# Kernel optimization log

Measured on AMD Instinct MI355X. Metric: run time of the kernel, lower is better.

The kernel has to match this reference:

```python
import jax, jax.numpy as jnp
import numpy as np

B, T, H, K = 256, 1024, 12, 6
EPS = 1e-5


def _lstm_layer(x, Wih, Whh, bih, bhh):
    # x: [B, T, H]; torch gate order i, f, g, o
    b = bih + bhh

    def step(carry, xt):
        h, c = carry
        gates = xt @ Wih.T + h @ Whh.T + b
        i, f, g, o = jnp.split(gates, 4, axis=-1)
        c = jax.nn.sigmoid(f) * c + jax.nn.sigmoid(i) * jnp.tanh(g)
        h = jax.nn.sigmoid(o) * jnp.tanh(c)
        return (h, c), h

    h0 = jnp.zeros((x.shape[0], H), x.dtype)
    (_, _), ys = jax.lax.scan(step, (h0, h0), jnp.swapaxes(x, 0, 1))
    return jnp.swapaxes(ys, 0, 1)


def _bn_per_step(x, gamma, beta):
    # BatchNorm1d applied independently at each timestep (training mode):
    # normalize over the batch axis for each (t, channel).
    mu = jnp.mean(x, axis=0, keepdims=True)
    var = jnp.mean((x - mu) ** 2, axis=0, keepdims=True)  # biased, as torch BN
    return gamma * (x - mu) * jax.lax.rsqrt(var + EPS) + beta


def setup_inputs() -> dict:
    key = jax.random.key(0)
    ks = jax.random.split(key, 12)
    s = 1.0 / np.sqrt(H)
    return {
        "mfcc": jax.random.normal(ks[0], (B, T, H), jnp.float32),
        "Wih": jax.random.uniform(ks[1], (3, 4 * H, H), jnp.float32, -s, s),
        "Whh": jax.random.uniform(ks[2], (3, 4 * H, H), jnp.float32, -s, s),
        "bih": jax.random.uniform(ks[3], (3, 4 * H), jnp.float32, -s, s),
        "bhh": jax.random.uniform(ks[4], (3, 4 * H), jnp.float32, -s, s),
        "fc1_w": jax.random.normal(ks[5], (64, H), jnp.float32) * 0.1,
        "fc1_b": jnp.zeros((64,), jnp.float32),
        "bn1_g": jnp.ones((64,), jnp.float32),
        "bn1_b": jnp.zeros((64,), jnp.float32),
        "fc2_w": jax.random.normal(ks[6], (128, 64), jnp.float32) * 0.1,
        "fc2_b": jnp.zeros((128,), jnp.float32),
        "bn2_g": jnp.ones((128,), jnp.float32),
        "bn2_b": jnp.zeros((128,), jnp.float32),
        "fc3_w": jax.random.normal(ks[7], (K, 128), jnp.float32) * 0.1,
        "fc3_b": jnp.zeros((K,), jnp.float32),
        "WI": jax.random.normal(ks[8], (K, H, H), jnp.float32) * 0.01,
    }


def reference(mfcc, Wih, Whh, bih, bhh, fc1_w, fc1_b, bn1_g, bn1_b,
              fc2_w, fc2_b, bn2_g, bn2_b, fc3_w, fc3_b, WI):
    # 3-layer LSTM, input/hidden = 12
    x = mfcc
    for l in range(3):
        x = _lstm_layer(x, Wih[l], Whh[l], bih[l], bhh[l])

    # per-timestep MLP with per-timestep BatchNorm (training-mode stats)
    h = jnp.einsum('bth,oh->bto', x, fc1_w) + fc1_b
    h = jax.nn.relu(_bn_per_step(h, bn1_g, bn1_b))
    h = jnp.einsum('bth,oh->bto', h, fc2_w) + fc2_b
    h = jax.nn.relu(_bn_per_step(h, bn2_g, bn2_b))
    lambs = jnp.einsum('bth,kh->btk', h, fc3_w) + fc3_b  # [B, T, K]

    # out[b,t] = mfcc[b,t] @ (I + sum_k lambs[b,t,k] * WI[k])
    #          = mfcc[b,t] + sum_k lambs[b,t,k] * (mfcc[b,t] @ WI[k])
    proj = jnp.einsum('btd,kde->btke', mfcc, WI)  # [B, T, K, 12]
    outs = mfcc + jnp.einsum('btk,btke->bte', lambs, proj)
    return outs[:, None, :, :]  # [B, 1, T, 12]
```

## Files before the change

### kernel.cpp

```cpp
#include <hip/hip_runtime.h>

#define T_LEN 1024
#define NBATCH 256
#define HDIM 12
#define PAIR_STRIDE 12288
#define X3_TB 16

typedef __fp16 fp16x2 __attribute__((ext_vector_type(2)));

#if __has_builtin(__builtin_amdgcn_exp2f)
#define EXP2F(x) __builtin_amdgcn_exp2f(x)
#else
#define EXP2F(x) exp2f(x)
#endif
#if __has_builtin(__builtin_amdgcn_rcpf)
#define RCPF(x) __builtin_amdgcn_rcpf(x)
#else
#define RCPF(x) (1.0f / (x))
#endif

#define KSIG -1.4426950408889634f
#define KTAN -2.8853900817779268f

__device__ __forceinline__ unsigned bperm(int byteidx, unsigned v) {
#if __has_builtin(__builtin_amdgcn_ds_bpermute)
  return (unsigned)__builtin_amdgcn_ds_bpermute(byteidx, (int)v);
#else
  return (unsigned)__shfl((int)v, byteidx >> 2, 64);
#endif
}

template <int Q>
__device__ __forceinline__ float qb(float v) {
#if __has_builtin(__builtin_amdgcn_mov_dpp)
  return __int_as_float(__builtin_amdgcn_mov_dpp(__float_as_int(v), Q * 0x55, 0xF, 0xF, true));
#else
  return __shfl(v, (threadIdx.x & ~3) | Q, 64);
#endif
}

__device__ __forceinline__ float row_shr4(float v) {
#if __has_builtin(__builtin_amdgcn_mov_dpp)
  return __int_as_float(__builtin_amdgcn_mov_dpp(__float_as_int(v), 0x114, 0xF, 0xF, true));
#else
  return __shfl(v, (threadIdx.x & 63) - 4, 64);
#endif
}

__device__ __forceinline__ float h16tof(unsigned short u) {
  union { unsigned short s; _Float16 h; } c; c.s = u; return (float)c.h;
}
__device__ __forceinline__ unsigned short f16bits(float f) {
  union { unsigned short s; _Float16 h; } c; c.h = (_Float16)f; return c.s;
}
__device__ __forceinline__ float h16lo(unsigned u) {
  union { unsigned short s; _Float16 h; } c; c.s = (unsigned short)(u & 0xffffu); return (float)c.h;
}
__device__ __forceinline__ float h16hi(unsigned u) {
  union { unsigned short s; _Float16 h; } c; c.s = (unsigned short)(u >> 16); return (float)c.h;
}
__device__ __forceinline__ unsigned pk16(float a, float b) {
#if __has_builtin(__builtin_amdgcn_cvt_pkrtz)
  fp16x2 h = __builtin_amdgcn_cvt_pkrtz(a, b);
  return __builtin_bit_cast(unsigned, h);
#else
  return (unsigned)f16bits(a) | ((unsigned)f16bits(b) << 16);
#endif
}

__device__ __forceinline__ float dot2acc(unsigned a, unsigned b, float c) {
#if __has_builtin(__builtin_amdgcn_fdot2)
  return __builtin_amdgcn_fdot2(__builtin_bit_cast(fp16x2, a), __builtin_bit_cast(fp16x2, b), c, false);
#else
  return fmaf(h16lo(a), h16lo(b), fmaf(h16hi(a), h16hi(b), c));
#endif
}

__device__ __forceinline__ float d3(const unsigned* w, const unsigned* h, float init) {
  float a = dot2acc(w[0], h[0], init);
  a = dot2acc(w[1], h[1], a);
  return dot2acc(w[2], h[2], a);
}

__device__ __forceinline__ float nlup(float av, float& cv, float c1, float c0) {
  float e = EXP2F(av);
  float n = fmaf(c1, RCPF(1.f + e), c0);
  float si = qb<0>(n), sf = qb<1>(n), tg = qb<2>(n), so = qb<3>(n);
  cv = fmaf(sf, cv, si * tg);
  float e2 = EXP2F(KTAN * cv);
  return so * fmaf(2.f, RCPF(1.f + e2), -1.f);
}
__device__ __forceinline__ unsigned packb(float hq, unsigned* hp) {
  float sh = row_shr4(hq);
  unsigned pkv = pk16(sh, hq);
  hp[0] = bperm(16, pkv);  hp[1] = bperm(48, pkv);  hp[2] = bperm(80, pkv);
  hp[3] = bperm(112, pkv); hp[4] = bperm(144, pkv); hp[5] = bperm(176, pkv);
  return pkv;
}

#define BARRIER_LGKM() asm volatile("s_waitcnt lgkmcnt(0)\n\ts_barrier" ::: "memory")

__global__ __launch_bounds__(64, 4) void pregate_kernel(
    const float* __restrict__ mfcc, const float* __restrict__ Wih,
    const float* __restrict__ bih, const float* __restrict__ bhh,
    const float* __restrict__ w2, const float* __restrict__ WI,
    const float* __restrict__ w1, unsigned* __restrict__ pg2,
    unsigned* __restrict__ w2pk, unsigned* __restrict__ wipk,
    unsigned* __restrict__ w1pk) {
  if (blockIdx.x >= 2048) {
    const int base = (blockIdx.x - 2048) * 64 + threadIdx.x;
    for (int i = base; i < 4096; i += 512) {
      int kp = i >> 7, c = i & 127;
      float2 v = ((const float2*)w2)[c * 32 + kp];
      w2pk[i] = pk16(v.x, v.y);
    }
    for (int i = base; i < 432; i += 512) {
      int k6 = i / 72, rem = i % 72, e = rem / 6, dp = rem % 6;
      wipk[i] = pk16(WI[k6 * 144 + (2 * dp) * HDIM + e],
                     WI[k6 * 144 + (2 * dp + 1) * HDIM + e]);
    }
    for (int i = base; i < 384; i += 512) {
      int ch = i / 6, dp = i % 6;
      float2 v = ((const float2*)w1)[ch * 6 + dp];
      w1pk[i] = pk16(v.x, v.y);
    }
    return;
  }
  const int b = blockIdx.x & 255;
  const int tc = blockIdx.x >> 8;
  const int lane = threadIdx.x;
  const int j = lane >> 2, q = lane & 3;
  const int jj = (j < HDIM) ? j : (HDIM - 1);
  const int g = q * HDIM + jj;
  const float kqv = (q == 2) ? KTAN : KSIG;
  float w[HDIM];
#pragma unroll
  for (int m = 0; m < HDIM; ++m) w[m] = kqv * Wih[g * HDIM + m];
  const float bias = kqv * (bih[g] + bhh[g]);
  const bool wr = (lane < 48);
  const float* xb = mfcc + (b * T_LEN + tc * 128) * HDIM;
  unsigned* out = pg2 + (unsigned)(tc * 64 * NBATCH + b) * 48 + lane;
  for (int tp = 0; tp < 64; ++tp) {
    float a0 = bias, a1 = bias;
#pragma unroll
    for (int d = 0; d < HDIM; ++d) {
      a0 = fmaf(w[d], xb[d], a0);
      a1 = fmaf(w[d], xb[HDIM + d], a1);
    }
    if (wr) *out = pk16(a0, a1);
    xb += 2 * HDIM;
    out += PAIR_STRIDE;
  }
}

__global__ __launch_bounds__(192, 1) void lstm3_kernel(
    const unsigned* __restrict__ pg2,
    const float* __restrict__ Wih, const float* __restrict__ Whh,
    const float* __restrict__ bih, const float* __restrict__ bhh,
    unsigned short* __restrict__ x3) {
  __shared__ __align__(16) unsigned ldsb[320];
  const int b = blockIdx.x;
  const int tid = threadIdx.x;
  const int wid = tid >> 6;
  const int lane = tid & 63;
  const int j = lane >> 2, q = lane & 3;
  const int jj = (j < HDIM) ? j : (HDIM - 1);
  const int g = q * HDIM + jj;
  const float kqv = (q == 2) ? KTAN : KSIG;
  const float c1c = (q == 2) ? 2.0f : 1.0f;
  const float c0c = (q == 2) ? -1.0f : 0.0f;

  const int row = (wid * 48 + g) * HDIM;
  unsigned wihp[6], whhp[6];
#pragma unroll
  for (int m = 0; m < 6; ++m) {
    wihp[m] = pk16(kqv * Wih[row + 2 * m], kqv * Wih[row + 2 * m + 1]);
    whhp[m] = pk16(kqv * Whh[row + 2 * m], kqv * Whh[row + 2 * m + 1]);
  }
  const float biasw = kqv * (bih[wid * 48 + g] + bhh[wid * 48 + g]);

  float cv = 0.f;
  unsigned hown[6] = {0, 0, 0, 0, 0, 0};

  const int grpi = lane >> 3;
  const bool wvalid = ((lane & 7) == 7) && (grpi < 6);
  const int wlayer = (wid == 0) ? 0 : 64;
  const int wsl = wvalid ? (wlayer + grpi) : (256 + lane);
  const int wst = wvalid ? 8 : 0;

  const int lane_src = (lane < 48) ? lane : (44 + (lane & 3));
  const char* pgbase = (const char*)(pg2 + (unsigned)b * 48);
  const unsigned PGB = PAIR_STRIDE * 4;
  const unsigned PGLIM = 513u * PGB;
  uint4 P0 = {0, 0, 0, 0}, P1 = P0, A0 = P0, A1 = P0;
  unsigned pg_upos = 0;
  if (wid == 0) {
    P0.x = *(const unsigned*)(pgbase + 0 * PGB + lane_src * 4);
    P0.y = *(const unsigned*)(pgbase + 1 * PGB + lane_src * 4);
    P0.z = *(const unsigned*)(pgbase + 2 * PGB + lane_src * 4);
    P0.w = *(const unsigned*)(pgbase + 3 * PGB + lane_src * 4);
    P1.x = *(const unsigned*)(pgbase + 4 * PGB + lane_src * 4);
    P1.y = *(const unsigned*)(pgbase + 5 * PGB + lane_src * 4);
    P1.z = *(const unsigned*)(pgbase + 6 * PGB + lane_src * 4);
    P1.w = *(const unsigned*)(pgbase + 7 * PGB + lane_src * 4);
    A0.x = *(const unsigned*)(pgbase + 8 * PGB + lane_src * 4);
    A0.y = *(const unsigned*)(pgbase + 9 * PGB + lane_src * 4);
    A0.z = *(const unsigned*)(pgbase + 10 * PGB + lane_src * 4);
    A0.w = *(const unsigned*)(pgbase + 11 * PGB + lane_src * 4);
    A1.x = *(const unsigned*)(pgbase + 12 * PGB + lane_src * 4);
    A1.y = *(const unsigned*)(pgbase + 13 * PGB + lane_src * 4);
    A1.z = *(const unsigned*)(pgbase + 14 * PGB + lane_src * 4);
    A1.w = *(const unsigned*)(pgbase + 15 * PGB + lane_src * 4);
    pg_upos = 16u * PGB;
  }

  char* x3b = (char*)(x3 + (unsigned)b * X3_TB);
  const int x3_loff = ((j & 1) && j < HDIM) ? (j - 1) * 2 : ((j < HDIM) ? 24 : 28);
  unsigned x3_upos = 0;
  const unsigned X3STEP = NBATCH * X3_TB * 2;

  auto l0_ss = [&](int par, uint4 P) {
    const int wpb = wvalid ? par * 128 : 0;
    const float pgf[8] = {h16lo(P.x), h16hi(P.x), h16lo(P.y), h16hi(P.y),
                          h16lo(P.z), h16hi(P.z), h16lo(P.w), h16hi(P.w)};
#pragma unroll
    for (int st = 0; st < 8; ++st) {
      float a = d3(whhp, hown, pgf[st]) + d3(whhp + 3, hown + 3, 0.f);
      float hq = nlup(a, cv, c1c, c0c);
      unsigned pkv = packb(hq, hown);
      ldsb[wpb + wsl + st * wst] = pkv;
    }
  };
  auto l1_ss = [&](int par) {
    const unsigned* rb = ldsb + (par ^ 1) * 128;
    unsigned hin[8][6];
#pragma unroll
    for (int st = 0; st < 8; ++st) {
      uint4 A = *(const uint4*)(rb + st * 8);
      uint2 B = *(const uint2*)(rb + st * 8 + 4);
      hin[st][0] = A.x; hin[st][1] = A.y; hin[st][2] = A.z;
      hin[st][3] = A.w; hin[st][4] = B.x; hin[st][5] = B.y;
    }
    float aI[8];
#pragma unroll
    for (int st = 0; st < 8; ++st)
      aI[st] = d3(wihp, hin[st], biasw) + d3(wihp + 3, hin[st] + 3, 0.f);
    const int wpb = wvalid ? par * 128 : 0;
#pragma unroll
    for (int st = 0; st < 8; ++st) {
      float a = aI[st] + (d3(whhp, hown, 0.f) + d3(whhp + 3, hown + 3, 0.f));
      float hq = nlup(a, cv, c1c, c0c);
      unsigned pkv = packb(hq, hown);
      ldsb[wpb + wsl + st * wst] = pkv;
    }
  };
  auto l2_ss = [&](int par) {
    const unsigned* rb = ldsb + (par ^ 1) * 128 + 64;
    unsigned hin[8][6];
#pragma unroll
    for (int st = 0; st < 8; ++st) {
      uint4 A = *(const uint4*)(rb + st * 8);
      uint2 B = *(const uint2*)(rb + st * 8 + 4);
      hin[st][0] = A.x; hin[st][1] = A.y; hin[st][2] = A.z;
      hin[st][3] = A.w; hin[st][4] = B.x; hin[st][5] = B.y;
    }
    float aI[8];
#pragma unroll
    for (int st = 0; st < 8; ++st)
      aI[st] = d3(wihp, hin[st], biasw) + d3(wihp + 3, hin[st] + 3, 0.f);
#pragma unroll
    for (int st = 0; st < 8; ++st) {
      float a = aI[st] + (d3(whhp, hown, 0.f) + d3(whhp + 3, hown + 3, 0.f));
      float hq = nlup(a, cv, c1c, c0c);
      unsigned pkv = packb(hq, hown);
      *(unsigned*)(x3b + x3_upos + st * X3STEP + x3_loff) = pkv;
    }
    x3_upos += 8 * X3STEP;
  };

  if (wid == 0) l0_ss(0, P0);
  BARRIER_LGKM();
  if (wid == 0) l0_ss(1, P1);
  else if (wid == 1) l1_ss(1);
  BARRIER_LGKM();
  for (int i = 0; i < 63; ++i) {
    uint4 N0 = {0, 0, 0, 0}, N1 = N0;
    if (wid == 0) {
      unsigned o0 = pg_upos, o1 = o0 + PGB, o2 = o0 + 2 * PGB, o3 = o0 + 3 * PGB;
      unsigned o4 = o0 + 4 * PGB, o5 = o0 + 5 * PGB, o6 = o0 + 6 * PGB, o7 = o0 + 7 * PGB;
      o0 = o0 > PGLIM ? PGLIM : o0; o1 = o1 > PGLIM ? PGLIM : o1;
      o2 = o2 > PGLIM ? PGLIM : o2; o3 = o3 > PGLIM ? PGLIM : o3;
      o4 = o4 > PGLIM ? PGLIM : o4; o5 = o5 > PGLIM ? PGLIM : o5;
      o6 = o6 > PGLIM ? PGLIM : o6; o7 = o7 > PGLIM ? PGLIM : o7;
      N0.x = *(const unsigned*)(pgbase + o0 + lane_src * 4);
      N0.y = *(const unsigned*)(pgbase + o1 + lane_src * 4);
      N0.z = *(const unsigned*)(pgbase + o2 + lane_src * 4);
      N0.w = *(const unsigned*)(pgbase + o3 + lane_src * 4);
      N1.x = *(const unsigned*)(pgbase + o4 + lane_src * 4);
      N1.y = *(const unsigned*)(pgbase + o5 + lane_src * 4);
      N1.z = *(const unsigned*)(pgbase + o6 + lane_src * 4);
      N1.w = *(const unsigned*)(pgbase + o7 + lane_src * 4);
      pg_upos += 8 * PGB;
      l0_ss(0, A0);
    } else if (wid == 1) {
      l1_ss(0);
    } else {
      l2_ss(0);
    }
    BARRIER_LGKM();
    if (wid == 0) l0_ss(1, A1);
    else if (wid == 1) l1_ss(1);
    else l2_ss(1);
    BARRIER_LGKM();
    if (wid == 0) { A0 = N0; A1 = N1; }
  }
  if (wid == 1) l1_ss(0);
  else if (wid == 2) l2_ss(0);
  BARRIER_LGKM();
  if (wid == 2) l2_ss(1);
}

__global__ __launch_bounds__(256, 2) void mlp_out_kernel(
    const unsigned short* __restrict__ x3, const float* __restrict__ mfcc,
    const unsigned* __restrict__ w1pk, const float* __restrict__ g1,
    const float* __restrict__ be1, const unsigned* __restrict__ w2pk,
    const float* __restrict__ g2, const float* __restrict__ be2,
    const float* __restrict__ w3, const float* __restrict__ b3,
    const unsigned* __restrict__ wipk, float* __restrict__ outp) {
  __shared__ __align__(16) unsigned char smem[53952];
  unsigned* h1p = (unsigned*)smem;
  unsigned* w2p = (unsigned*)(smem + 32768);
  float* p3 = (float*)smem;
  float* stp = (float*)(smem + 49152);
  float* scsh = (float*)(smem + 51200);
  unsigned* wis = (unsigned*)(smem + 52224);

  const int t = blockIdx.x;
  const int tid = threadIdx.x;

  for (int i = tid; i < 1024; i += 256)
    ((uint4*)w2p)[i] = ((const uint4*)w2pk)[i];
  for (int i = tid; i < 432; i += 256) wis[i] = wipk[i];

  {
    const unsigned short* xp = x3 + t * (NBATCH * X3_TB) + tid * X3_TB;
    uint2 u0 = ((const uint2*)xp)[0];
    uint2 u1 = ((const uint2*)xp)[1];
    uint2 u2 = ((const uint2*)xp)[2];
    const unsigned u[6] = {u0.x, u0.y, u1.x, u1.y, u2.x, u2.y};
#pragma unroll 4
    for (int kp = 0; kp < 32; ++kp) {
      const unsigned* wp = w1pk + kp * 12;
      float a0 = dot2acc(wp[0], u[0], 0.f);
      float a1 = dot2acc(wp[6], u[0], 0.f);
#pragma unroll
      for (int dp = 1; dp < 6; ++dp) {
        a0 = dot2acc(wp[dp], u[dp], a0);
        a1 = dot2acc(wp[6 + dp], u[dp], a1);
      }
      h1p[kp * 256 + tid] = pk16(a0, a1);
    }
  }
  __syncthreads();

  {
    const int kp = tid & 31, seg = tid >> 5;
    const uint4* rp = (const uint4*)(h1p + kp * 256 + seg * 32);
    float sl = 0.f, sh = 0.f, ql = 0.f, qh = 0.f;
#pragma unroll
    for (int i = 0; i < 8; ++i) {
      uint4 v = rp[(i + kp) & 7];
      float f0 = h16lo(v.x), f1 = h16hi(v.x), f2 = h16lo(v.y), f3 = h16hi(v.y);
      float f4 = h16lo(v.z), f5 = h16hi(v.z), f6 = h16lo(v.w), f7 = h16hi(v.w);
      sl += (f0 + f2) + (f4 + f6);
      sh += (f1 + f3) + (f5 + f7);
      ql = fmaf(f0, f0, ql); ql = fmaf(f2, f2, ql); ql = fmaf(f4, f4, ql); ql = fmaf(f6, f6, ql);
      qh = fmaf(f1, f1, qh); qh = fmaf(f3, f3, qh); qh = fmaf(f5, f5, qh); qh = fmaf(f7, f7, qh);
    }
    sl += __shfl_xor(sl, 32, 64); sh += __shfl_xor(sh, 32, 64);
    ql += __shfl_xor(ql, 32, 64); qh += __shfl_xor(qh, 32, 64);
    if ((tid & 63) < 32) {
      float* sp = stp + kp * 16 + (tid >> 6) * 4;
      sp[0] = sl; sp[1] = sh; sp[2] = ql; sp[3] = qh;
    }
  }
  __syncthreads();
  if (tid < 64) {
    const int kp = tid >> 1, par = tid & 1;
    float s = 0.f, qq = 0.f;
#pragma unroll
    for (int w = 0; w < 4; ++w) {
      s += stp[kp * 16 + w * 4 + par];
      qq += stp[kp * 16 + w * 4 + 2 + par];
    }
    const int ch = 2 * kp + par;
    float mu = s * (1.f / 256.f);
    float var = fmaf(-mu, mu, qq * (1.f / 256.f));
    float sc = g1[ch] * rsqrtf(var + 1e-5f);
    scsh[ch * 2] = sc;
    scsh[ch * 2 + 1] = fmaf(-sc, mu, be1[ch]);
  }
  __syncthreads();
  {
    unsigned* cp = h1p + tid;
#pragma unroll 8
    for (int kp = 0; kp < 32; ++kp) {
      unsigned v = cp[kp * 256];
      float fl = fmaxf(fmaf(scsh[kp * 4 + 0], h16lo(v), scsh[kp * 4 + 1]), 0.f);
      float fh = fmaxf(fmaf(scsh[kp * 4 + 2], h16hi(v), scsh[kp * 4 + 3]), 0.f);
      cp[kp * 256] = pk16(fl, fh);
    }
  }
  __syncthreads();

  const int tb = tid & 31, tc2 = tid >> 5;
  const int b0 = tb * 8, cc0 = tc2 * 16;
  float acc[8][16];
#pragma unroll
  for (int bi = 0; bi < 8; ++bi)
#pragma unroll
    for (int ci = 0; ci < 16; ++ci) acc[bi][ci] = 0.f;

  for (int kp = 0; kp < 32; ++kp) {
    const unsigned* hrow = h1p + kp * 256 + b0;
    uint4 a01 = ((const uint4*)hrow)[0];
    uint4 a23 = ((const uint4*)hrow)[1];
    const unsigned ap[8] = {a01.x, a01.y, a01.z, a01.w, a23.x, a23.y, a23.z, a23.w};
    const unsigned* wrow = w2p + kp * 128 + cc0;
#pragma unroll
    for (int wq = 0; wq < 4; ++wq) {
      uint4 wv = ((const uint4*)wrow)[wq];
      const unsigned ww[4] = {wv.x, wv.y, wv.z, wv.w};
#pragma unroll
      for (int bi = 0; bi < 8; ++bi)
#pragma unroll
        for (int cj = 0; cj < 4; ++cj)
          acc[bi][wq * 4 + cj] = dot2acc(ap[bi], ww[cj], acc[bi][wq * 4 + cj]);
    }
  }

  {
    float sv[16], qv[16];
#pragma unroll
    for (int ci = 0; ci < 16; ++ci) {
      float s = 0.f, sq = 0.f;
#pragma unroll
      for (int bi = 0; bi < 8; ++bi) {
        s += acc[bi][ci];
        sq = fmaf(acc[bi][ci], acc[bi][ci], sq);
      }
      sv[ci] = s; qv[ci] = sq;
    }
#pragma unroll
    for (int m = 1; m <= 16; m <<= 1) {
#pragma unroll
      for (int ci = 0; ci < 16; ++ci) {
        sv[ci] += __shfl_xor(sv[ci], m, 64);
        qv[ci] += __shfl_xor(qv[ci], m, 64);
      }
    }
    if (tb == 0) {
#pragma unroll
      for (int ci = 0; ci < 16; ++ci) {
        stp[(cc0 + ci) * 2] = sv[ci];
        stp[(cc0 + ci) * 2 + 1] = qv[ci];
      }
    }
  }
  __syncthreads();
  if (tid < 128) {
    float mu = stp[tid * 2] * (1.f / 256.f);
    float var = fmaf(-mu, mu, stp[tid * 2 + 1] * (1.f / 256.f));
    float sc = g2[tid] * rsqrtf(var + 1e-5f);
    scsh[tid * 2] = sc;
    scsh[tid * 2 + 1] = fmaf(-sc, mu, be2[tid]);
  }
  __syncthreads();

  {
    float lam[8][6];
#pragma unroll
    for (int bi = 0; bi < 8; ++bi)
#pragma unroll
      for (int k6 = 0; k6 < 6; ++k6) lam[bi][k6] = 0.f;
#pragma unroll
    for (int ci = 0; ci < 16; ++ci) {
      const float sc = scsh[(cc0 + ci) * 2], shv = scsh[(cc0 + ci) * 2 + 1];
      float wv6[6];
#pragma unroll
      for (int k6 = 0; k6 < 6; ++k6) wv6[k6] = w3[k6 * 128 + cc0 + ci];
#pragma unroll
      for (int bi = 0; bi < 8; ++bi) {
        float v = fmaxf(fmaf(sc, acc[bi][ci], shv), 0.f);
#pragma unroll
        for (int k6 = 0; k6 < 6; ++k6)
          lam[bi][k6] = fmaf(v, wv6[k6], lam[bi][k6]);
      }
    }
#pragma unroll
    for (int bi = 0; bi < 8; ++bi)
#pragma unroll
      for (int k6 = 0; k6 < 6; ++k6)
        p3[(tc2 * 256 + b0 + bi) * 6 + k6] = lam[bi][k6];
  }
  __syncthreads();

  {
    float lm[6];
#pragma unroll
    for (int k6 = 0; k6 < 6; ++k6) lm[k6] = b3[k6];
#pragma unroll
    for (int tcc = 0; tcc < 8; ++tcc)
#pragma unroll
      for (int k6 = 0; k6 < 6; ++k6) lm[k6] += p3[(tcc * 256 + tid) * 6 + k6];

    const float4* mp = (const float4*)(mfcc + (tid * T_LEN + t) * HDIM);
    float4 m0 = mp[0], m1 = mp[1], m2 = mp[2];
    const float x[HDIM] = {m0.x, m0.y, m0.z, m0.w, m1.x, m1.y,
                           m1.z, m1.w, m2.x, m2.y, m2.z, m2.w};
    unsigned xpk[6];
#pragma unroll
    for (int dp = 0; dp < 6; ++dp) xpk[dp] = pk16(x[2 * dp], x[2 * dp + 1]);
    float o[HDIM];
#pragma unroll
    for (int e = 0; e < HDIM; ++e) o[e] = x[e];
#pragma unroll
    for (int k6 = 0; k6 < 6; ++k6) {
      const unsigned* wrow = wis + k6 * 72;
#pragma unroll
      for (int e = 0; e < HDIM; ++e) {
        float s = dot2acc(xpk[0], wrow[e * 6 + 0], 0.f);
        s = dot2acc(xpk[1], wrow[e * 6 + 1], s);
        s = dot2acc(xpk[2], wrow[e * 6 + 2], s);
        s = dot2acc(xpk[3], wrow[e * 6 + 3], s);
        s = dot2acc(xpk[4], wrow[e * 6 + 4], s);
        s = dot2acc(xpk[5], wrow[e * 6 + 5], s);
        o[e] = fmaf(lm[k6], s, o[e]);
      }
    }
    float4* op4 = (float4*)(outp + (tid * T_LEN + t) * HDIM);
    op4[0] = make_float4(o[0], o[1], o[2], o[3]);
    op4[1] = make_float4(o[4], o[5], o[6], o[7]);
    op4[2] = make_float4(o[8], o[9], o[10], o[11]);
  }
}

extern "C" void kernel_launch(void* const* d_in, const int* in_sizes, int n_in,
                              void* d_out, int out_size, void* d_ws, size_t ws_size,
                              hipStream_t stream) {
  const float* mfcc = (const float*)d_in[0];
  const float* Wih = (const float*)d_in[1];
  const float* Whh = (const float*)d_in[2];
  const float* bih = (const float*)d_in[3];
  const float* bhh = (const float*)d_in[4];
  const float* w1 = (const float*)d_in[5];
  const float* g1 = (const float*)d_in[7];
  const float* be1 = (const float*)d_in[8];
  const float* w2 = (const float*)d_in[9];
  const float* g2 = (const float*)d_in[11];
  const float* be2 = (const float*)d_in[12];
  const float* w3 = (const float*)d_in[13];
  const float* b3 = (const float*)d_in[14];
  const float* WI = (const float*)d_in[15];

  unsigned* pg2 = (unsigned*)d_ws;
  unsigned short* x3 = (unsigned short*)((char*)d_ws + 25264128);
  unsigned* w2pk = (unsigned*)((char*)d_ws + 33652736);
  unsigned* wipk = (unsigned*)((char*)d_ws + 33669120);
  unsigned* w1pk = (unsigned*)((char*)d_ws + 33670848);
  float* out = (float*)d_out;

  hipLaunchKernelGGL(pregate_kernel, dim3(2056), dim3(64), 0, stream,
                     mfcc, Wih, bih, bhh, w2, WI, w1, pg2, w2pk, wipk, w1pk);
  hipLaunchKernelGGL(lstm3_kernel, dim3(NBATCH), dim3(192), 0, stream,
                     pg2, Wih, Whh, bih, bhh, x3);
  hipLaunchKernelGGL(mlp_out_kernel, dim3(T_LEN), dim3(256), 0, stream,
                     x3, mfcc, w1pk, g1, be1, w2pk, g2, be2, w3, b3, wipk, out);
}
```

Measured before the change: 235.3 us.

## Split fc2 output channels into two passes to cut registers and raise occupancy

The fc2 GEMM in the MLP kernel is split into two passes of 64 channels, so each thread holds an 8x8 accumulator tile instead of 8x16. This lowers register pressure and lets launch bounds ask for three blocks per CU. fc2 weights are now read straight from global memory instead of being staged in LDS, and the lambda partials are pre-reduced with a cross-lane shuffle and stored as fp16 to shrink shared memory. The price is extra barriers and BN-stat rounds per pass, global-memory weight reads, and fp16 rounding of the partial lambda sums.

```diff
diff --git a/kernel.cpp b/kernel.cpp
--- a/kernel.cpp
+++ b/kernel.cpp
@@ -320,26 +320,23 @@
   if (wid == 2) l2_ss(1);
 }
 
-__global__ __launch_bounds__(256, 2) void mlp_out_kernel(
+__global__ __launch_bounds__(256, 3) void mlp_out_kernel(
     const unsigned short* __restrict__ x3, const float* __restrict__ mfcc,
     const unsigned* __restrict__ w1pk, const float* __restrict__ g1,
     const float* __restrict__ be1, const unsigned* __restrict__ w2pk,
     const float* __restrict__ g2, const float* __restrict__ be2,
     const float* __restrict__ w3, const float* __restrict__ b3,
     const unsigned* __restrict__ wipk, float* __restrict__ outp) {
-  __shared__ __align__(16) unsigned char smem[53952];
+  __shared__ __align__(16) unsigned char smem[49856];
   unsigned* h1p = (unsigned*)smem;
-  unsigned* w2p = (unsigned*)(smem + 32768);
-  float* p3 = (float*)smem;
-  float* stp = (float*)(smem + 49152);
-  float* scsh = (float*)(smem + 51200);
-  unsigned* wis = (unsigned*)(smem + 52224);
+  unsigned* p3h = (unsigned*)(smem + 32768);
+  float* stp = (float*)(smem + 45056);
+  float* scsh = (float*)(smem + 47104);
+  unsigned* wis = (unsigned*)(smem + 48128);
 
   const int t = blockIdx.x;
   const int tid = threadIdx.x;
 
-  for (int i = tid; i < 1024; i += 256)
-    ((uint4*)w2p)[i] = ((const uint4*)w2pk)[i];
   for (int i = tid; i < 432; i += 256) wis[i] = wipk[i];
 
   {
@@ -361,7 +358,7 @@
       h1p[kp * 256 + tid] = pk16(a0, a1);
     }
   }
-  __syncthreads();
+  BARRIER_LGKM();
 
   {
     const int kp = tid & 31, seg = tid >> 5;
@@ -384,7 +381,7 @@
       sp[0] = sl; sp[1] = sh; sp[2] = ql; sp[3] = qh;
     }
   }
-  __syncthreads();
+  BARRIER_LGKM();
   if (tid < 64) {
     const int kp = tid >> 1, par = tid & 1;
     float s = 0.f, qq = 0.f;
@@ -400,7 +397,7 @@
     scsh[ch * 2] = sc;
     scsh[ch * 2 + 1] = fmaf(-sc, mu, be1[ch]);
   }
-  __syncthreads();
+  BARRIER_LGKM();
   {
     unsigned* cp = h1p + tid;
 #pragma unroll 8
@@ -411,109 +408,128 @@
       cp[kp * 256] = pk16(fl, fh);
     }
   }
-  __syncthreads();
+  BARRIER_LGKM();
 
   const int tb = tid & 31, tc2 = tid >> 5;
-  const int b0 = tb * 8, cc0 = tc2 * 16;
-  float acc[8][16];
-#pragma unroll
-  for (int bi = 0; bi < 8; ++bi)
-#pragma unroll
-    for (int ci = 0; ci < 16; ++ci) acc[bi][ci] = 0.f;
-
-  for (int kp = 0; kp < 32; ++kp) {
-    const unsigned* hrow = h1p + kp * 256 + b0;
-    uint4 a01 = ((const uint4*)hrow)[0];
-    uint4 a23 = ((const uint4*)hrow)[1];
-    const unsigned ap[8] = {a01.x, a01.y, a01.z, a01.w, a23.x, a23.y, a23.z, a23.w};
-    const unsigned* wrow = w2p + kp * 128 + cc0;
-#pragma unroll
-    for (int wq = 0; wq < 4; ++wq) {
-      uint4 wv = ((const uint4*)wrow)[wq];
-      const unsigned ww[4] = {wv.x, wv.y, wv.z, wv.w};
+  const int b0 = tb * 8;
+  float lm[6];
+#pragma unroll
+  for (int k6 = 0; k6 < 6; ++k6) lm[k6] = b3[k6];
+
+  for (int p = 0; p < 2; ++p) {
+    const int c0 = p * 64 + tc2 * 8;
+    float acc[8][8];
+#pragma unroll
+    for (int bi = 0; bi < 8; ++bi)
+#pragma unroll
+      for (int ci = 0; ci < 8; ++ci) acc[bi][ci] = 0.f;
+
+    for (int kp = 0; kp < 32; ++kp) {
+      const unsigned* hrow = h1p + kp * 256 + b0;
+      uint4 a01 = ((const uint4*)hrow)[0];
+      uint4 a23 = ((const uint4*)hrow)[1];
+      const unsigned ap[8] = {a01.x, a01.y, a01.z, a01.w, a23.x, a23.y, a23.z, a23.w};
+      const unsigned* wrow = w2pk + kp * 128 + c0;
+      uint4 wv0 = ((const uint4*)wrow)[0];
+      uint4 wv1 = ((const uint4*)wrow)[1];
+      const unsigned ww[8] = {wv0.x, wv0.y, wv0.z, wv0.w, wv1.x, wv1.y, wv1.z, wv1.w};
 #pragma unroll
       for (int bi = 0; bi < 8; ++bi)
 #pragma unroll
-        for (int cj = 0; cj < 4; ++cj)
-          acc[bi][wq * 4 + cj] = dot2acc(ap[bi], ww[cj], acc[bi][wq * 4 + cj]);
-    }
+        for (int ci = 0; ci < 8; ++ci)
+          acc[bi][ci] = dot2acc(ap[bi], ww[ci], acc[bi][ci]);
+    }
+
+    {
+      float sv[8], qv[8];
+#pragma unroll
+      for (int ci = 0; ci < 8; ++ci) {
+        float s = 0.f, sq = 0.f;
+#pragma unroll
+        for (int bi = 0; bi < 8; ++bi) {
+          s += acc[bi][ci];
+          sq = fmaf(acc[bi][ci], acc[bi][ci], sq);
+        }
+        sv[ci] = s; qv[ci] = sq;
+      }
+#pragma unroll
+      for (int m = 1; m <= 16; m <<= 1) {
+#pragma unroll
+        for (int ci = 0; ci < 8; ++ci) {
+          sv[ci] += __shfl_xor(sv[ci], m, 64);
+          qv[ci] += __shfl_xor(qv[ci], m, 64);
+        }
+      }
+      if (tb == 0) {
+#pragma unroll
+        for (int ci = 0; ci < 8; ++ci) {
+          stp[(c0 + ci) * 2] = sv[ci];
+          stp[(c0 + ci) * 2 + 1] = qv[ci];
+        }
+      }
+    }
+    BARRIER_LGKM();
+    if (tid < 64) {
+      const int ch = p * 64 + tid;
+      float mu = stp[ch * 2] * (1.f / 256.f);
+      float var = fmaf(-mu, mu, stp[ch * 2 + 1] * (1.f / 256.f));
+      float sc = g2[ch] * rsqrtf(var + 1e-5f);
+      scsh[ch * 2] = sc;
+      scsh[ch * 2 + 1] = fmaf(-sc, mu, be2[ch]);
+    }
+    BARRIER_LGKM();
+
+    {
+      float lam[8][6];
+#pragma unroll
+      for (int bi = 0; bi < 8; ++bi)
+#pragma unroll
+        for (int k6 = 0; k6 < 6; ++k6) lam[bi][k6] = 0.f;
+#pragma unroll
+      for (int ci = 0; ci < 8; ++ci) {
+        const float sc = scsh[(c0 + ci) * 2], shv = scsh[(c0 + ci) * 2 + 1];
+        float wv6[6];
+#pragma unroll
+        for (int k6 = 0; k6 < 6; ++k6) wv6[k6] = w3[k6 * 128 + c0 + ci];
+#pragma unroll
+        for (int bi = 0; bi < 8; ++bi) {
+          float v = fmaxf(fmaf(sc, acc[bi][ci], shv), 0.f);
+#pragma unroll
+          for (int k6 = 0; k6 < 6; ++k6)
+            lam[bi][k6] = fmaf(v, wv6[k6], lam[bi][k6]);
+        }
+      }
+#pragma unroll
+      for (int bi = 0; bi < 8; ++bi)
+#pragma unroll
+        for (int k6 = 0; k6 < 6; ++k6)
+          lam[bi][k6] += __shfl_xor(lam[bi][k6], 32, 64);
+      if ((tc2 & 1) == 0) {
+        const int gg = tc2 >> 1;
+#pragma unroll
+        for (int bi = 0; bi < 8; ++bi) {
+          p3h[gg * 768 + (b0 + bi) * 3 + 0] = pk16(lam[bi][0], lam[bi][1]);
+          p3h[gg * 768 + (b0 + bi) * 3 + 1] = pk16(lam[bi][2], lam[bi][3]);
+          p3h[gg * 768 + (b0 + bi) * 3 + 2] = pk16(lam[bi][4], lam[bi][5]);
+        }
+      }
+    }
+    BARRIER_LGKM();
+    {
+#pragma unroll
+      for (int gg = 0; gg < 4; ++gg) {
+#pragma unroll
+        for (int d = 0; d < 3; ++d) {
+          unsigned v = p3h[gg * 768 + tid * 3 + d];
+          lm[2 * d] += h16lo(v);
+          lm[2 * d + 1] += h16hi(v);
+        }
+      }
+    }
+    BARRIER_LGKM();
   }
 
   {
-    float sv[16], qv[16];
-#pragma unroll
-    for (int ci = 0; ci < 16; ++ci) {
-      float s = 0.f, sq = 0.f;
-#pragma unroll
-      for (int bi = 0; bi < 8; ++bi) {
-        s += acc[bi][ci];
-        sq = fmaf(acc[bi][ci], acc[bi][ci], sq);
-      }
-      sv[ci] = s; qv[ci] = sq;
-    }
-#pragma unroll
-    for (int m = 1; m <= 16; m <<= 1) {
-#pragma unroll
-      for (int ci = 0; ci < 16; ++ci) {
-        sv[ci] += __shfl_xor(sv[ci], m, 64);
-        qv[ci] += __shfl_xor(qv[ci], m, 64);
-      }
-    }
-    if (tb == 0) {
-#pragma unroll
-      for (int ci = 0; ci < 16; ++ci) {
-        stp[(cc0 + ci) * 2] = sv[ci];
-        stp[(cc0 + ci) * 2 + 1] = qv[ci];
-      }
-    }
-  }
-  __syncthreads();
-  if (tid < 128) {
-    float mu = stp[tid * 2] * (1.f / 256.f);
-    float var = fmaf(-mu, mu, stp[tid * 2 + 1] * (1.f / 256.f));
-    float sc = g2[tid] * rsqrtf(var + 1e-5f);
-    scsh[tid * 2] = sc;
-    scsh[tid * 2 + 1] = fmaf(-sc, mu, be2[tid]);
-  }
-  __syncthreads();
-
-  {
-    float lam[8][6];
-#pragma unroll
-    for (int bi = 0; bi < 8; ++bi)
-#pragma unroll
-      for (int k6 = 0; k6 < 6; ++k6) lam[bi][k6] = 0.f;
-#pragma unroll
-    for (int ci = 0; ci < 16; ++ci) {
-      const float sc = scsh[(cc0 + ci) * 2], shv = scsh[(cc0 + ci) * 2 + 1];
-      float wv6[6];
-#pragma unroll
-      for (int k6 = 0; k6 < 6; ++k6) wv6[k6] = w3[k6 * 128 + cc0 + ci];
-#pragma unroll
-      for (int bi = 0; bi < 8; ++bi) {
-        float v = fmaxf(fmaf(sc, acc[bi][ci], shv), 0.f);
-#pragma unroll
-        for (int k6 = 0; k6 < 6; ++k6)
-          lam[bi][k6] = fmaf(v, wv6[k6], lam[bi][k6]);
-      }
-    }
-#pragma unroll
-    for (int bi = 0; bi < 8; ++bi)
-#pragma unroll
-      for (int k6 = 0; k6 < 6; ++k6)
-        p3[(tc2 * 256 + b0 + bi) * 6 + k6] = lam[bi][k6];
-  }
-  __syncthreads();
-
-  {
-    float lm[6];
-#pragma unroll
-    for (int k6 = 0; k6 < 6; ++k6) lm[k6] = b3[k6];
-#pragma unroll
-    for (int tcc = 0; tcc < 8; ++tcc)
-#pragma unroll
-      for (int k6 = 0; k6 < 6; ++k6) lm[k6] += p3[(tcc * 256 + tid) * 6 + k6];
-
     const float4* mp = (const float4*)(mfcc + (tid * T_LEN + t) * HDIM);
     float4 m0 = mp[0], m1 = mp[1], m2 = mp[2];
     const float x[HDIM] = {m0.x, m0.y, m0.z, m0.w, m1.x, m1.y,
```

Measured after the change: 253.2 us. 1.08x slower.
